# Optimization experiments

Measured on AMD Instinct MI355X. Metric: run time of the kernel, lower is better.

The kernel has to match this reference:

```python
import jax, jax.numpy as jnp
import numpy as np

STRIDE = 1
KSIZE = 3
DEMOD = True


def _conv_single(xi, wi, pad):
    # xi: [C,H,W], wi: [O,C,k,k] -> [O,H,W]
    out = jax.lax.conv_general_dilated(
        xi[None], wi, window_strides=(STRIDE, STRIDE),
        padding=[(pad, pad), (pad, pad)],
        dimension_numbers=("NCHW", "OIHW", "NCHW"))
    return out[0]


def setup_inputs() -> dict:
    key = jax.random.key(0)
    ks = jax.random.split(key, 6)
    B, Cin, Cout, S, H, W = 8, 512, 512, 512, 64, 64
    return {
        "x": jax.random.normal(ks[0], (B, Cin, H, W), jnp.float32),
        "y": jax.random.normal(ks[1], (B, S), jnp.float32),
        "affine_w": jax.random.normal(ks[2], (Cin, S), jnp.float32) * 0.02,
        "affine_b": jax.random.normal(ks[3], (Cin,), jnp.float32) * 0.02,
        "weight": jax.random.normal(ks[4], (Cout, Cin, KSIZE, KSIZE), jnp.float32) * 0.05,
        "bias": jax.random.normal(ks[5], (1, Cout, 1, 1), jnp.float32) * 0.02,
    }


def reference(x, y, affine_w, affine_b, weight, bias):
    B, _, H, W = x.shape
    style_dim = affine_w.shape[1]
    coef = 1.0 / np.sqrt(style_dim)  # ELR: gain / sqrt(fan_in)
    # style modulation scale per input channel: [B, Cin]
    s = (y * coef) @ affine_w.T + affine_b + 1.0
    # per-sample weights: [B, O, I, k, k]
    w = weight[None, :, :, :, :] * s[:, None, :, None, None]
    if DEMOD:
        d = jax.lax.rsqrt(jnp.sum(w * w, axis=(2, 3, 4), keepdims=True) + 1e-4)
        w = w * d
    pad = ((H - 1) * (STRIDE - 1) + (KSIZE - 1)) // 2
    out = jax.vmap(lambda xi, wi: _conv_single(xi, wi, pad))(x, w)  # [B,O,H,W]
    return out + bias
```

## Files before the change

### kernel.cpp

```cpp
#include <hip/hip_runtime.h>

typedef __attribute__((ext_vector_type(8))) short short8;
typedef __attribute__((ext_vector_type(4))) float floatx4;
typedef unsigned short u16;
typedef unsigned int u32;

#define NB 8
#define CI 512
#define CO 512
#define HH 64
#define WW 64
#define HP 66
#define WP 66
#define BK 64

__device__ __forceinline__ u16 f2bf(float f) {
  u32 u = __builtin_bit_cast(u32, f);
  u += 0x7fffu + ((u >> 16) & 1u);
  return (u16)(u >> 16);
}

__device__ __forceinline__ void gload16(const void* g, void* l) {
  __builtin_amdgcn_global_load_lds(
      (const __attribute__((address_space(1))) unsigned int*)g,
      (__attribute__((address_space(3))) unsigned int*)l, 16, 0, 0);
}

__global__ __launch_bounds__(256) void k_prep1(
    const float* __restrict__ y, const float* __restrict__ aw,
    const float* __restrict__ ab, float* __restrict__ s,
    const float* __restrict__ wt, float* __restrict__ wsum,
    u16* __restrict__ wbv)
{
  if (blockIdx.x < 1024) {
    const int wid = blockIdx.x * 4 + (threadIdx.x >> 6);
    const int lane = threadIdx.x & 63;
    const int b = wid >> 9, i = wid & 511;
    float sum = 0.f;
    #pragma unroll
    for (int j = 0; j < 8; ++j) {
      const int k = lane + (j << 6);
      sum += y[b * CI + k] * aw[i * CI + k];
    }
    #pragma unroll
    for (int off = 32; off; off >>= 1) sum += __shfl_xor(sum, off);
    if (lane == 0) s[wid] = sum * 0.044194173824159216f + ab[i] + 1.0f;
  } else {
    const int idx = (blockIdx.x - 1024) * 256 + threadIdx.x;
    const int i = idx & 511;
    const int o = idx >> 9;
    const float* p = wt + (size_t)idx * 9;
    float v[9];
    float sum = 0.f;
    #pragma unroll
    for (int t = 0; t < 9; ++t) { v[t] = p[t]; sum += v[t] * v[t]; }
    wsum[idx] = sum;
    #pragma unroll
    for (int t = 0; t < 9; ++t) wbv[(((o * 9 + t) << 9) | i)] = f2bf(v[t]);
  }
}

__global__ __launch_bounds__(256) void k_xfd(
    const float* __restrict__ x, const float* __restrict__ s,
    u16* __restrict__ xs, const float* __restrict__ wsum,
    float* __restrict__ d)
{
  __shared__ __align__(16) u16 lds[64 * 72];
  if (blockIdx.x >= 4096) {
    const int wid = (blockIdx.x - 4096) * 4 + (threadIdx.x >> 6);
    const int lane = threadIdx.x & 63;
    const int b = wid >> 9, o = wid & 511;
    float sum = 0.f;
    #pragma unroll
    for (int j = 0; j < 8; ++j) {
      const int i = lane + (j << 6);
      const float sv = s[b * CI + i];
      sum += wsum[o * CI + i] * sv * sv;
    }
    #pragma unroll
    for (int off = 32; off; off >>= 1) sum += __shfl_xor(sum, off);
    if (lane == 0) d[wid] = rsqrtf(sum + 1e-4f);
    return;
  }
  const int blk = blockIdx.x;
  const int ic = blk & 7;
  const int h = (blk >> 3) & 63;
  const int b = blk >> 9;
  const int i0 = ic << 6;
  const int t = threadIdx.x;
  const int w = t & 63;
  const int i4 = t >> 6;
  #pragma unroll
  for (int p = 0; p < 16; ++p) {
    const int ii = i4 + (p << 2);
    const float xv = x[((size_t)(b * CI + i0 + ii) * HH + h) * WW + w];
    const float sv = s[b * CI + i0 + ii];
    lds[w * 72 + ii] = f2bf(xv * sv);
  }
  const uint4 z4 = {0u, 0u, 0u, 0u};
  if (t < 16) {
    const int wside = (t < 8) ? 0 : 65;
    const int q = t & 7;
    *(uint4*)&xs[((size_t)(b * HP + h + 1) * WP + wside) * CI + i0 + (q << 3)] = z4;
  }
  if (h == 0) {
    for (int idx = t; idx < 2 * 66 * 8; idx += 256) {
      const int row = (idx < 528) ? 0 : 65;
      const int rem = (idx < 528) ? idx : idx - 528;
      const int wz = rem >> 3;
      const int q = rem & 7;
      *(uint4*)&xs[((size_t)(b * HP + row) * WP + wz) * CI + i0 + (q << 3)] = z4;
    }
  }
  __syncthreads();
  const int w2 = t >> 2;
  const int q = t & 3;
  const uint4* src = (const uint4*)&lds[w2 * 72 + (q << 4)];
  const uint4 v0 = src[0];
  const uint4 v1 = src[1];
  u16* dst = xs + ((size_t)(b * HP + h + 1) * WP + (w2 + 1)) * CI + i0 + (q << 4);
  *(uint4*)dst = v0;
  *((uint4*)dst + 1) = v1;
}

__global__ __launch_bounds__(512, 2) void k_conv(
    const u16* __restrict__ xs, const u16* __restrict__ wb,
    const float* __restrict__ dmod, const float* __restrict__ bias,
    float* __restrict__ out)
{
  __shared__ __align__(16) u16 lA[2 * 16384];
  __shared__ __align__(16) u16 lB[2 * 16384];

  const int blk = blockIdx.x;
  const int nt = blk & 15;
  const int mt = (blk >> 4) & 1;
  const int b  = blk >> 5;
  const int ob = mt << 8;
  const int p0 = nt << 8;

  const int tid = threadIdx.x;
  const int wid = tid >> 6;
  const int lane = tid & 63;
  const int col = lane & 15;
  const int k8  = lane >> 4;
  const int wr  = wid >> 2;
  const int wc  = wid & 3;

  const int lr = lane >> 3;
  const int ls = lane & 7;
  const int swz = ls ^ lr;

  u32 aoff[4], boff[4], ldst[4];
  #pragma unroll
  for (int h2 = 0; h2 < 4; ++h2) {
    const int rowBase = ((h2 >> 1) << 7) + (wid << 4) + ((h2 & 1) << 3);
    const int rowIdx = rowBase + lr;
    aoff[h2] = (u32)((ob + rowIdx) * 4608 + (swz << 3));
    const int p = p0 + rowIdx;
    boff[h2] = (u32)(((b * HP + (p >> 6)) * WP + (p & 63)) * 512 + (swz << 3));
    ldst[h2] = (u32)(rowBase << 6);
  }

  const u32 sA0 = (u32)(((0 + k8) ^ (col & 7)) << 3);
  const u32 sA1 = (u32)(((4 + k8) ^ (col & 7)) << 3);
  const u32 aRead = (u32)((((wr << 7) + col) << 6));
  const u32 bRead = (u32)((((wc << 6) + col) << 6));

  floatx4 acc[8][4];
  #pragma unroll
  for (int m = 0; m < 8; ++m)
    #pragma unroll
    for (int n = 0; n < 4; ++n)
      acc[m][n] = (floatx4){0.f, 0.f, 0.f, 0.f};

  short8 a0[4][2], b0[2][2], b1[2][2];

#define SA(TILE, H, BUF) do {                                                 \
    const u32 at_ = (u32)((TILE) << 6);                                       \
    gload16(wb + aoff[(H)*2+0] + at_, &lA[((BUF) << 14) + ldst[(H)*2+0]]);    \
    gload16(wb + aoff[(H)*2+1] + at_, &lA[((BUF) << 14) + ldst[(H)*2+1]]);    \
  } while (0)

#define SB(TILE, H, BUF) do {                                                 \
    const int t_ = (TILE);                                                    \
    const int tap_ = t_ >> 3;                                                 \
    const int kh_ = tap_ / 3;                                                 \
    const int kw_ = tap_ - kh_ * 3;                                           \
    const u32 bt_ = (u32)(((kh_ * WP + kw_) << 9) + ((t_ & 7) << 6));         \
    gload16(xs + boff[(H)*2+0] + bt_, &lB[((BUF) << 14) + ldst[(H)*2+0]]);    \
    gload16(xs + boff[(H)*2+1] + bt_, &lB[((BUF) << 14) + ldst[(H)*2+1]]);    \
  } while (0)

#define READ_A(PA, MH) do {                                                   \
    _Pragma("unroll")                                                         \
    for (int mq = 0; mq < 4; ++mq) {                                          \
      a0[mq][0] = *(const short8*)((PA) + (MH) * 4096 + mq * 1024 + sA0);     \
      a0[mq][1] = *(const short8*)((PA) + (MH) * 4096 + mq * 1024 + sA1);     \
    }                                                                         \
  } while (0)

#define READ_B(PB, NH, BV) do {                                               \
    _Pragma("unroll")                                                         \
    for (int nq = 0; nq < 2; ++nq) {                                          \
      BV[nq][0] = *(const short8*)((PB) + (NH) * 2048 + nq * 1024 + sA0);     \
      BV[nq][1] = *(const short8*)((PB) + (NH) * 2048 + nq * 1024 + sA1);     \
    }                                                                         \
  } while (0)

#define MFMA_Q(MH, NH, BV) do {                                               \
    _Pragma("unroll")                                                         \
    for (int kk = 0; kk < 2; ++kk)                                            \
      _Pragma("unroll")                                                       \
      for (int nq = 0; nq < 2; ++nq)                                          \
        _Pragma("unroll")                                                     \
        for (int mq = 0; mq < 4; ++mq)                                        \
          acc[(MH)*4+mq][(NH)*2+nq] = __builtin_amdgcn_mfma_f32_16x16x32_bf16(\
              a0[mq][kk], BV[nq][kk], acc[(MH)*4+mq][(NH)*2+nq], 0, 0, 0);    \
  } while (0)

#define SBAR __builtin_amdgcn_s_barrier()
#define SCH0 __builtin_amdgcn_sched_barrier(0)
#define PRI1 __builtin_amdgcn_s_setprio(1)
#define PRI0 __builtin_amdgcn_s_setprio(0)
#define LGKM0 do { asm volatile("s_waitcnt lgkmcnt(0)" ::: "memory"); SCH0; } while (0)

#define TILE4(T, C, MODE) do {                                                \
    const u16* pA  = lA + ((C) << 14) + aRead;                                \
    const u16* pB  = lB + ((C) << 14) + bRead;                                \
    const u16* pBn = lB + ((1 - (C)) << 14) + bRead;                          \
                           \
    READ_A(pA, 0);                                                            \
    SBAR; LGKM0; PRI1; MFMA_Q(0, 0, b0); PRI0; SBAR;                          \
                                                       \
    READ_B(pB, 1, b1);                                                        \
    SBAR; LGKM0; PRI1; MFMA_Q(0, 1, b1); PRI0; SBAR;                          \
        \
    READ_A(pA, 1);                                                            \
    SCH0; if (MODE == 2) { SB((T) + 2, 0, C); SB((T) + 2, 1, C); }            \
    SBAR; LGKM0; PRI1; MFMA_Q(1, 1, b1); PRI0; SBAR;                          \
      \
    SCH0; if (MODE == 2) { SA((T) + 2, 0, C); SA((T) + 2, 1, C); }            \
    SBAR; LGKM0; PRI1; MFMA_Q(1, 0, b0); PRI0;                                \
    if (MODE == 2)      asm volatile("s_waitcnt vmcnt(8)" ::: "memory");      \
    else if (MODE == 1) asm volatile("s_waitcnt vmcnt(0)" ::: "memory");      \
    SCH0;                                                                     \
    if (MODE >= 1) READ_B(pBn, 0, b0);                                        \
    SBAR;                                                                     \
  } while (0)

  SB(0, 0, 0); SB(0, 1, 0); SA(0, 0, 0); SA(0, 1, 0);
  SB(1, 0, 1); SB(1, 1, 1); SA(1, 0, 1); SA(1, 1, 1);
  asm volatile("s_waitcnt vmcnt(8)" ::: "memory");
  SCH0;
  SBAR;
  {
    const u16* pB0 = lB + bRead;
    READ_B(pB0, 0, b0);
  }

  for (int j = 0; j < 35; ++j) {
    TILE4(2 * j,     0, 2);
    TILE4(2 * j + 1, 1, 2);
  }
  TILE4(70, 0, 1);
  TILE4(71, 1, 0);

#undef SA
#undef SB
#undef READ_A
#undef READ_B
#undef MFMA_Q
#undef TILE4
#undef SBAR
#undef SCH0
#undef PRI1
#undef PRI0
#undef LGKM0

  #pragma unroll
  for (int m = 0; m < 8; ++m) {
    #pragma unroll
    for (int r = 0; r < 4; ++r) {
      const int o = ob + (wr << 7) + (m << 4) + (k8 << 2) + r;
      const float dm = dmod[b * CO + o];
      const float bs = bias[o];
      float* po = out + (((size_t)(b * CO + o)) << 12) + p0 + (wc << 6);
      #pragma unroll
      for (int n = 0; n < 4; ++n)
        po[(n << 4) + col] = acc[m][n][r] * dm + bs;
    }
  }
}

extern "C" void kernel_launch(void* const* d_in, const int* in_sizes, int n_in,
                              void* d_out, int out_size, void* d_ws, size_t ws_size,
                              hipStream_t stream) {
  const float* x    = (const float*)d_in[0];
  const float* y    = (const float*)d_in[1];
  const float* aw   = (const float*)d_in[2];
  const float* ab   = (const float*)d_in[3];
  const float* wt   = (const float*)d_in[4];
  const float* bias = (const float*)d_in[5];
  float* out = (float*)d_out;

  char* ws = (char*)d_ws;
  const size_t XS_BYTES = (size_t)NB * HP * WP * CI * 2;
  const size_t WB_BYTES = (size_t)CO * 9 * CI * 2;
  const size_t WS_BYTES = (size_t)CO * CI * 4;
  u16* xsb    = (u16*)ws;
  u16* wbuf   = (u16*)(ws + XS_BYTES);
  float* wsum = (float*)(ws + XS_BYTES + WB_BYTES);
  float* sbuf = (float*)(ws + XS_BYTES + WB_BYTES + WS_BYTES);
  float* dbuf = sbuf + NB * CI;

  k_prep1<<<dim3(2048), dim3(256), 0, stream>>>(y, aw, ab, sbuf, wt, wsum, wbuf);
  k_xfd  <<<dim3(5120), dim3(256), 0, stream>>>(x, sbuf, xsb, wsum, dbuf);
  k_conv <<<dim3(256), dim3(512), 0, stream>>>(xsb, wbuf, dbuf, bias, out);
}
```

Before: 158.7 us.

## Load conv weights directly from global into MFMA fragment registers, dropping A LDS staging

```diff
diff --git a/kernel.cpp b/kernel.cpp
--- a/kernel.cpp
+++ b/kernel.cpp
@@ -12,7 +12,6 @@
 #define WW 64
 #define HP 66
 #define WP 66
-#define BK 64
 
 __device__ __forceinline__ u16 f2bf(float f) {
   u32 u = __builtin_bit_cast(u32, f);
@@ -55,8 +54,14 @@
     #pragma unroll
     for (int t = 0; t < 9; ++t) { v[t] = p[t]; sum += v[t] * v[t]; }
     wsum[idx] = sum;
-    #pragma unroll
-    for (int t = 0; t < 9; ++t) wbv[(((o * 9 + t) << 9) | i)] = f2bf(v[t]);
+    const int g = o >> 4, col = o & 15;
+    const int kk = (i >> 5) & 1, k8 = (i >> 3) & 3, j = i & 7;
+    const int lanepart = (((k8 << 4) | col) << 3) + j;
+    #pragma unroll
+    for (int t9 = 0; t9 < 9; ++t9) {
+      const int t = t9 * 8 + (i >> 6);
+      wbv[((((t * 32 + g) * 2 + kk) << 9) | lanepart)] = f2bf(v[t9]);
+    }
   }
 }
 
@@ -124,19 +129,18 @@
 }
 
 __global__ __launch_bounds__(512, 2) void k_conv(
-    const u16* __restrict__ xs, const u16* __restrict__ wb,
+    const u16* __restrict__ xs, const u16* __restrict__ wbf,
     const float* __restrict__ dmod, const float* __restrict__ bias,
     float* __restrict__ out)
 {
-  __shared__ __align__(16) u16 lA[2 * 16384];
   __shared__ __align__(16) u16 lB[2 * 16384];
 
   const int blk = blockIdx.x;
   const int nt = blk & 15;
   const int mt = (blk >> 4) & 1;
   const int b  = blk >> 5;
+  const int p0 = nt << 8;
   const int ob = mt << 8;
-  const int p0 = nt << 8;
 
   const int tid = threadIdx.x;
   const int wid = tid >> 6;
@@ -146,16 +150,18 @@
   const int wr  = wid >> 2;
   const int wc  = wid & 3;
 
+  const int gbase = (mt << 4) + (wr << 3);
+  const u32 lane8 = (u32)(lane << 3);
+
   const int lr = lane >> 3;
   const int ls = lane & 7;
   const int swz = ls ^ lr;
 
-  u32 aoff[4], boff[4], ldst[4];
+  u32 boff[4], ldst[4];
   #pragma unroll
   for (int h2 = 0; h2 < 4; ++h2) {
     const int rowBase = ((h2 >> 1) << 7) + (wid << 4) + ((h2 & 1) << 3);
     const int rowIdx = rowBase + lr;
-    aoff[h2] = (u32)((ob + rowIdx) * 4608 + (swz << 3));
     const int p = p0 + rowIdx;
     boff[h2] = (u32)(((b * HP + (p >> 6)) * WP + (p & 63)) * 512 + (swz << 3));
     ldst[h2] = (u32)(rowBase << 6);
@@ -163,7 +169,6 @@
 
   const u32 sA0 = (u32)(((0 + k8) ^ (col & 7)) << 3);
   const u32 sA1 = (u32)(((4 + k8) ^ (col & 7)) << 3);
-  const u32 aRead = (u32)((((wr << 7) + col) << 6));
   const u32 bRead = (u32)((((wc << 6) + col) << 6));
 
   floatx4 acc[8][4];
@@ -173,12 +178,13 @@
     for (int n = 0; n < 4; ++n)
       acc[m][n] = (floatx4){0.f, 0.f, 0.f, 0.f};
 
-  short8 a0[4][2], b0[2][2], b1[2][2];
-
-#define SA(TILE, H, BUF) do {                                                 \
-    const u32 at_ = (u32)((TILE) << 6);                                       \
-    gload16(wb + aoff[(H)*2+0] + at_, &lA[((BUF) << 14) + ldst[(H)*2+0]]);    \
-    gload16(wb + aoff[(H)*2+1] + at_, &lA[((BUF) << 14) + ldst[(H)*2+1]]);    \
+  short8 aK0[8], aK1[8], b0[2][2], b1[2][2];
+
+#define GLBA(SET, T, KK) do {                                                 \
+    _Pragma("unroll")                                                         \
+    for (int mq = 0; mq < 8; ++mq)                                            \
+      SET[mq] = *(const short8*)(wbf +                                        \
+          (((u32)((T) * 32 + gbase + mq) * 2 + (KK)) << 9) + lane8);          \
   } while (0)
 
 #define SB(TILE, H, BUF) do {                                                 \
@@ -191,14 +197,6 @@
     gload16(xs + boff[(H)*2+1] + bt_, &lB[((BUF) << 14) + ldst[(H)*2+1]]);    \
   } while (0)
 
-#define READ_A(PA, MH) do {                                                   \
-    _Pragma("unroll")                                                         \
-    for (int mq = 0; mq < 4; ++mq) {                                          \
-      a0[mq][0] = *(const short8*)((PA) + (MH) * 4096 + mq * 1024 + sA0);     \
-      a0[mq][1] = *(const short8*)((PA) + (MH) * 4096 + mq * 1024 + sA1);     \
-    }                                                                         \
-  } while (0)
-
 #define READ_B(PB, NH, BV) do {                                               \
     _Pragma("unroll")                                                         \
     for (int nq = 0; nq < 2; ++nq) {                                          \
@@ -207,75 +205,70 @@
     }                                                                         \
   } while (0)
 
-#define MFMA_Q(MH, NH, BV) do {                                               \
+#define MFMA32(ASET, KK) do {                                                 \
     _Pragma("unroll")                                                         \
-    for (int kk = 0; kk < 2; ++kk)                                            \
+    for (int nq = 0; nq < 2; ++nq)                                            \
       _Pragma("unroll")                                                       \
-      for (int nq = 0; nq < 2; ++nq)                                          \
-        _Pragma("unroll")                                                     \
-        for (int mq = 0; mq < 4; ++mq)                                        \
-          acc[(MH)*4+mq][(NH)*2+nq] = __builtin_amdgcn_mfma_f32_16x16x32_bf16(\
-              a0[mq][kk], BV[nq][kk], acc[(MH)*4+mq][(NH)*2+nq], 0, 0, 0);    \
+      for (int mq = 0; mq < 8; ++mq)                                          \
+        acc[mq][nq] = __builtin_amdgcn_mfma_f32_16x16x32_bf16(                \
+            ASET[mq], b0[nq][KK], acc[mq][nq], 0, 0, 0);                      \
+    _Pragma("unroll")                                                         \
+    for (int nq = 0; nq < 2; ++nq)                                            \
+      _Pragma("unroll")                                                       \
+      for (int mq = 0; mq < 8; ++mq)                                          \
+        acc[mq][2 + nq] = __builtin_amdgcn_mfma_f32_16x16x32_bf16(            \
+            ASET[mq], b1[nq][KK], acc[mq][2 + nq], 0, 0, 0);                  \
   } while (0)
 
 #define SBAR __builtin_amdgcn_s_barrier()
 #define SCH0 __builtin_amdgcn_sched_barrier(0)
 #define PRI1 __builtin_amdgcn_s_setprio(1)
 #define PRI0 __builtin_amdgcn_s_setprio(0)
-#define LGKM0 do { asm volatile("s_waitcnt lgkmcnt(0)" ::: "memory"); SCH0; } while (0)
-
-#define TILE4(T, C, MODE) do {                                                \
-    const u16* pA  = lA + ((C) << 14) + aRead;                                \
-    const u16* pB  = lB + ((C) << 14) + bRead;                                \
-    const u16* pBn = lB + ((1 - (C)) << 14) + bRead;                          \
-                           \
-    READ_A(pA, 0);                                                            \
-    SBAR; LGKM0; PRI1; MFMA_Q(0, 0, b0); PRI0; SBAR;                          \
-                                                       \
+
+#define TILE2(T, C, MODE) do {                                                \
+    const u16* pB = lB + ((C) << 14) + bRead;                                 \
+                  \
+    READ_B(pB, 0, b0);                                                        \
     READ_B(pB, 1, b1);                                                        \
-    SBAR; LGKM0; PRI1; MFMA_Q(0, 1, b1); PRI0; SBAR;                          \
-        \
-    READ_A(pA, 1);                                                            \
-    SCH0; if (MODE == 2) { SB((T) + 2, 0, C); SB((T) + 2, 1, C); }            \
-    SBAR; LGKM0; PRI1; MFMA_Q(1, 1, b1); PRI0; SBAR;                          \
-      \
-    SCH0; if (MODE == 2) { SA((T) + 2, 0, C); SA((T) + 2, 1, C); }            \
-    SBAR; LGKM0; PRI1; MFMA_Q(1, 0, b0); PRI0;                                \
-    if (MODE == 2)      asm volatile("s_waitcnt vmcnt(8)" ::: "memory");      \
-    else if (MODE == 1) asm volatile("s_waitcnt vmcnt(0)" ::: "memory");      \
+    GLBA(aK1, T, 1);                                                          \
     SCH0;                                                                     \
-    if (MODE >= 1) READ_B(pBn, 0, b0);                                        \
+    PRI1; MFMA32(aK0, 0); PRI0;                                               \
+    asm volatile("s_waitcnt lgkmcnt(0)" ::: "memory");                        \
+    SCH0;                                                                     \
     SBAR;                                                                     \
-  } while (0)
-
-  SB(0, 0, 0); SB(0, 1, 0); SA(0, 0, 0); SA(0, 1, 0);
-  SB(1, 0, 1); SB(1, 1, 1); SA(1, 0, 1); SA(1, 1, 1);
-  asm volatile("s_waitcnt vmcnt(8)" ::: "memory");
+                \
+    if (MODE == 2) { SB((T) + 2, 0, C); SB((T) + 2, 1, C); }                  \
+    if (MODE >= 1) GLBA(aK0, (T) + 1, 0);                                     \
+    SCH0;                                                                     \
+    PRI1; MFMA32(aK1, 1); PRI0;                                               \
+    if (MODE == 2)      asm volatile("s_waitcnt vmcnt(12)" ::: "memory");     \
+    else if (MODE == 1) asm volatile("s_waitcnt vmcnt(8)" ::: "memory");      \
+    SCH0;                                                                     \
+  } while (0)
+
+  SB(0, 0, 0); SB(0, 1, 0);
+  SB(1, 0, 1); SB(1, 1, 1);
+  GLBA(aK0, 0, 0);
+  asm volatile("s_waitcnt vmcnt(12)" ::: "memory");
   SCH0;
   SBAR;
-  {
-    const u16* pB0 = lB + bRead;
-    READ_B(pB0, 0, b0);
-  }
 
   for (int j = 0; j < 35; ++j) {
-    TILE4(2 * j,     0, 2);
-    TILE4(2 * j + 1, 1, 2);
-  }
-  TILE4(70, 0, 1);
-  TILE4(71, 1, 0);
-
-#undef SA
+    TILE2(2 * j,     0, 2);
+    TILE2(2 * j + 1, 1, 2);
+  }
+  TILE2(70, 0, 1);
+  TILE2(71, 1, 0);
+
+#undef GLBA
 #undef SB
-#undef READ_A
 #undef READ_B
-#undef MFMA_Q
-#undef TILE4
+#undef MFMA32
+#undef TILE2
 #undef SBAR
 #undef SCH0
 #undef PRI1
 #undef PRI0
-#undef LGKM0
 
   #pragma unroll
   for (int m = 0; m < 8; ++m) {
@@ -305,7 +298,7 @@
 
   char* ws = (char*)d_ws;
   const size_t XS_BYTES = (size_t)NB * HP * WP * CI * 2;
-  const size_t WB_BYTES = (size_t)CO * 9 * CI * 2;
+  const size_t WB_BYTES = (size_t)72 * 32 * 2 * 512 * 2;
   const size_t WS_BYTES = (size_t)CO * CI * 4;
   u16* xsb    = (u16*)ws;
   u16* wbuf   = (u16*)(ws + XS_BYTES);
```

Measured after the change: 165.3 us. +4.2%, slower.
